# Optimization experiments

Measured on AMD Instinct MI355X. Metric: run time of the kernel, lower is better.

The kernel has to match this reference:

```python
import jax, jax.numpy as jnp
import numpy as np

N_NODES = 10000
N_EDGES = 160000
IN_CH = 1030
HID = 256
HEADS = 4
OUT_CH = 49
NEG_SLOPE = 0.2
EPS = 1e-5


def setup_inputs() -> dict:
    key = jax.random.key(0)
    ks = jax.random.split(key, 20)
    HC = HID * HEADS  # 1024
    inp = {
        "x": jax.random.normal(ks[0], (N_NODES, IN_CH), dtype=jnp.float32),
        "edge_index": jax.random.randint(ks[1], (2, N_EDGES), 0, N_NODES, dtype=jnp.int64),
        # conv1 (GATv2): lin_l (source), lin_r (target), att, out bias
        "c1_wl": jax.random.normal(ks[2], (IN_CH, HC), dtype=jnp.float32) * 0.03,
        "c1_bl": jnp.zeros((HC,), dtype=jnp.float32),
        "c1_wr": jax.random.normal(ks[3], (IN_CH, HC), dtype=jnp.float32) * 0.03,
        "c1_br": jnp.zeros((HC,), dtype=jnp.float32),
        "c1_att": jax.random.normal(ks[4], (HEADS, HID), dtype=jnp.float32) * 0.06,
        "c1_bias": jnp.zeros((HC,), dtype=jnp.float32),
        # norm1 (per-node LayerNorm over channels)
        "ln1_w": jnp.ones((HC,), dtype=jnp.float32),
        "ln1_b": jnp.zeros((HC,), dtype=jnp.float32),
        # conv2
        "c2_wl": jax.random.normal(ks[5], (HC, HC), dtype=jnp.float32) * 0.03,
        "c2_bl": jnp.zeros((HC,), dtype=jnp.float32),
        "c2_wr": jax.random.normal(ks[6], (HC, HC), dtype=jnp.float32) * 0.03,
        "c2_br": jnp.zeros((HC,), dtype=jnp.float32),
        "c2_att": jax.random.normal(ks[7], (HEADS, HID), dtype=jnp.float32) * 0.06,
        "c2_bias": jnp.zeros((HC,), dtype=jnp.float32),
        # norm2
        "ln2_w": jnp.ones((HC,), dtype=jnp.float32),
        "ln2_b": jnp.zeros((HC,), dtype=jnp.float32),
        # classifier: Linear(HC, HID) -> ELU -> Linear(HID, OUT_CH)
        "cls_w1": jax.random.normal(ks[8], (HC, HID), dtype=jnp.float32) * 0.03,
        "cls_b1": jnp.zeros((HID,), dtype=jnp.float32),
        "cls_w2": jax.random.normal(ks[9], (HID, OUT_CH), dtype=jnp.float32) * 0.06,
        "cls_b2": jnp.zeros((OUT_CH,), dtype=jnp.float32),
    }
    return inp


def gatv2_conv(x, src, dst, wl, bl, wr, br, att, bias, n_nodes):
    """PyG GATv2Conv, concat heads. src/dst include self loops."""
    H, C = att.shape
    xl = (x @ wl + bl).reshape(-1, H, C)  # source transform [N,H,C]
    xr = (x @ wr + br).reshape(-1, H, C)  # target transform [N,H,C]
    m = xl[src] + xr[dst]                  # [E,H,C] gather + add
    e = jnp.einsum("ehc,hc->eh", jax.nn.leaky_relu(m, NEG_SLOPE), att)  # [E,H]
    # segment softmax over destination node
    emax = jax.ops.segment_max(e, dst, num_segments=n_nodes)
    p = jnp.exp(e - emax[dst])
    denom = jax.ops.segment_sum(p, dst, num_segments=n_nodes)
    alpha = p / (denom[dst] + 1e-16)       # [E,H]
    out = jax.ops.segment_sum(xl[src] * alpha[:, :, None], dst, num_segments=n_nodes)
    return out.reshape(n_nodes, H * C) + bias


def layer_norm(x, w, b):
    mu = jnp.mean(x, axis=-1, keepdims=True)
    var = jnp.var(x, axis=-1, keepdims=True)
    return (x - mu) / jnp.sqrt(var + EPS) * w + b


def reference(x, edge_index, c1_wl, c1_bl, c1_wr, c1_br, c1_att, c1_bias,
              ln1_w, ln1_b, c2_wl, c2_bl, c2_wr, c2_br, c2_att, c2_bias,
              ln2_w, ln2_b, cls_w1, cls_b1, cls_w2, cls_b2):
    n = x.shape[0]
    loops = jnp.arange(n, dtype=edge_index.dtype)
    src = jnp.concatenate([edge_index[0], loops])  # add_self_loops=True
    dst = jnp.concatenate([edge_index[1], loops])

    h = gatv2_conv(x, src, dst, c1_wl, c1_bl, c1_wr, c1_br, c1_att, c1_bias, n)
    h = jax.nn.elu(layer_norm(h, ln1_w, ln1_b))
    # dropout: identity at inference
    h = gatv2_conv(h, src, dst, c2_wl, c2_bl, c2_wr, c2_br, c2_att, c2_bias, n)
    h = jax.nn.elu(layer_norm(h, ln2_w, ln2_b))
    h = jax.nn.elu(h @ cls_w1 + cls_b1)
    return h @ cls_w2 + cls_b2  # [N, 49]
```

## Files before the change

### kernel.cpp

```cpp
#include <hip/hip_runtime.h>
#include <stdint.h>

#define N_NODES 10000
#define N_EDGES 160000
#define E_TOT   170000
#define IN_CH   1030
#define HC      1024
#define OUT_CH  49
#define NEG_SLOPE 0.2f
#define LN_EPS 1e-5f

#define MPAD  10112
#define K1PAD 1088

typedef __attribute__((ext_vector_type(8))) __bf16 bf16x8;
typedef __attribute__((ext_vector_type(4))) float floatx4;
typedef __attribute__((ext_vector_type(2))) float floatx2;

static __device__ __forceinline__ unsigned short f2bf(float f) {
  union { float f; uint32_t u; } v; v.f = f;
  uint32_t u = v.u;
  u += 0x7fffu + ((u >> 16) & 1u);
  return (unsigned short)(u >> 16);
}
static __device__ __forceinline__ floatx2 unpk2(uint32_t u) {
  union { uint32_t i; float f; } a, b;
  a.i = u << 16; b.i = u & 0xffff0000u;
  floatx2 r; r.x = a.f; r.y = b.f; return r;
}
static __device__ __forceinline__ floatx2 max2(floatx2 a, floatx2 b) {
  floatx2 r; r.x = fmaxf(a.x, b.x); r.y = fmaxf(a.y, b.y); return r;
}


__global__ void cast_x_kernel(const float* __restrict__ x, unsigned short* __restrict__ xa) {
  int idx = blockIdx.x * 256 + threadIdx.x;
  if (idx >= N_NODES * K1PAD) return;
  int m = idx / K1PAD, k = idx - m * K1PAD;
  float v = (k < IN_CH) ? x[m * IN_CH + k] : 0.f;
  xa[idx] = f2bf(v);
}

__global__ void transpose_cast_kernel(const float* __restrict__ wa, const float* __restrict__ wb,
                                      int split, int lda, int ldb,
                                      int Kvalid, int Kout, unsigned short* __restrict__ out) {
  __shared__ float tile[32][33];
  int n0 = blockIdx.x * 32, k0 = blockIdx.y * 32;
  int tx = threadIdx.x, ty = threadIdx.y;
#pragma unroll
  for (int i = 0; i < 4; i++) {
    int k = k0 + ty + i * 8;
    int n = n0 + tx;
    float v = 0.f;
    if (k < Kvalid) v = (n < split) ? wa[(size_t)k * lda + n] : wb[(size_t)k * ldb + (n - split)];
    tile[ty + i * 8][tx] = v;
  }
  __syncthreads();
#pragma unroll
  for (int i = 0; i < 4; i++) {
    int n = n0 + ty + i * 8;
    int k = k0 + tx;
    out[(size_t)n * Kout + k] = f2bf(tile[tx][ty + i * 8]);
  }
}

__global__ void w2t_kernel(const float* __restrict__ w2, float* __restrict__ out) {
  int o = blockIdx.x;
  int k = threadIdx.x;
  out[o * 256 + k] = w2[k * OUT_CH + o];
}


__global__ void count_kernel(const int* __restrict__ dstArr, int* __restrict__ counts) {
  int e = blockIdx.x * 256 + threadIdx.x;
  if (e >= E_TOT) return;
  int d = (e < N_EDGES) ? dstArr[e] : (e - N_EDGES);
  atomicAdd(&counts[d], 1);
}

__global__ __launch_bounds__(256) void scan_kernel(const int* __restrict__ counts,
                                                   int* __restrict__ rstart) {
  __shared__ int sm[256];
  int t = threadIdx.x;
  int b0 = t * 40;
  int b1 = b0 + 40; if (b1 > N_NODES) b1 = N_NODES; if (b0 > N_NODES) b0 = N_NODES;
  int s = 0;
  for (int i = b0; i < b1; i++) s += counts[i];
  sm[t] = s; __syncthreads();
  for (int st = 1; st < 256; st <<= 1) {
    int add = (t >= st) ? sm[t - st] : 0;
    __syncthreads();
    sm[t] += add;
    __syncthreads();
  }
  int run = sm[t] - s;
  for (int i = b0; i < b1; i++) { rstart[i] = run; run += counts[i]; }
  if (t == 255) rstart[N_NODES] = run;
}

__global__ void scatter_kernel(const int* __restrict__ srcArr, const int* __restrict__ dstArr,
                               const int* __restrict__ row_start,
                               int* __restrict__ cursor, int* __restrict__ csrsrc) {
  int e = blockIdx.x * 256 + threadIdx.x;
  if (e >= E_TOT) return;
  int d, sv;
  if (e < N_EDGES) { d = dstArr[e]; sv = srcArr[e]; }
  else { d = e - N_EDGES; sv = d; }
  int pos = atomicAdd(&cursor[d], 1);
  csrsrc[row_start[d] + pos] = sv;
}

template <int MODE>
__global__ __launch_bounds__(256) void gemm_bf16(
    const unsigned short* __restrict__ A, const unsigned short* __restrict__ Bt,
    float* __restrict__ Cf, unsigned short* __restrict__ Cb,
    const float* __restrict__ blo, const float* __restrict__ bhi,
    int M, int K, int ldc, int bsplit)
{
  __shared__ __align__(16) unsigned short As[128 * 64];
  __shared__ __align__(16) unsigned short Bs[128 * 64];
  const int t = threadIdx.x;
  const int w = t >> 6, lane = t & 63;
  const int tile_n = blockIdx.x * 128, tile_m = blockIdx.y * 128;

  floatx4 acc[4][4] = {};

  const int q = w * 64 + lane;
  const int row0 = q >> 3;
  const int gj = (q & 7) ^ (row0 & 7);
  const unsigned short* gA0 = A  + (size_t)(tile_m + row0) * K + gj * 8;
  const unsigned short* gB0 = Bt + (size_t)(tile_n + row0) * K + gj * 8;

  const int wm = (w >> 1) * 64, wn = (w & 1) * 64;
  const int lrow = lane & 15, cg0 = (lane >> 4);
  const int sw = lrow & 7;

  for (int k0 = 0; k0 < K; k0 += 64) {
#pragma unroll
    for (int p = 0; p < 4; p++) {
      __builtin_amdgcn_global_load_lds(
          (const __attribute__((address_space(1))) void*)(gA0 + (size_t)p * 32 * K),
          (__attribute__((address_space(3))) void*)(As + p * 2048 + w * 512), 16, 0, 0);
      __builtin_amdgcn_global_load_lds(
          (const __attribute__((address_space(1))) void*)(gB0 + (size_t)p * 32 * K),
          (__attribute__((address_space(3))) void*)(Bs + p * 2048 + w * 512), 16, 0, 0);
    }
    gA0 += 64; gB0 += 64;
    __syncthreads();
#pragma unroll
    for (int h = 0; h < 2; h++) {
      const int sc = (h * 4 + cg0) ^ sw;
      bf16x8 a[4], b[4];
#pragma unroll
      for (int mi = 0; mi < 4; mi++)
        a[mi] = *(const bf16x8*)(As + (wm + mi * 16 + lrow) * 64 + sc * 8);
#pragma unroll
      for (int ni = 0; ni < 4; ni++)
        b[ni] = *(const bf16x8*)(Bs + (wn + ni * 16 + lrow) * 64 + sc * 8);
#pragma unroll
      for (int mi = 0; mi < 4; mi++)
#pragma unroll
        for (int ni = 0; ni < 4; ni++)
          acc[mi][ni] = __builtin_amdgcn_mfma_f32_16x16x32_bf16(a[mi], b[ni], acc[mi][ni], 0, 0, 0);
    }
    __syncthreads();
  }

  const int rbase = (lane >> 4) * 4;
#pragma unroll
  for (int mi = 0; mi < 4; mi++) {
#pragma unroll
    for (int r = 0; r < 4; r++) {
      int m = tile_m + wm + mi * 16 + rbase + r;
      if (m >= M) continue;
#pragma unroll
      for (int ni = 0; ni < 4; ni++) {
        int n = tile_n + wn + ni * 16 + lrow;
        float v = acc[mi][ni][r] + (n < bsplit ? blo[n] : bhi[n - bsplit]);
        if (MODE == 0) {
          Cf[(size_t)m * ldc + n] = v;
        } else if (MODE == 1) {
          Cf[(size_t)m * ldc + n] = v > 0.f ? v : expm1f(v);
        } else {
          Cb[(size_t)m * 2048 + n] = f2bf(v);
        }
      }
    }
  }
}


__global__ __launch_bounds__(256) void gat_ln_kernel(
    const unsigned short* __restrict__ xlr,
    const float* __restrict__ att,
    const int* __restrict__ csrsrc, const int* __restrict__ rstart,
    const float* __restrict__ bias,
    const float* __restrict__ lnw, const float* __restrict__ lnb,
    unsigned short* __restrict__ out)
{
  const int d = blockIdx.x;
  const int t = threadIdx.x;
  const int lane = t & 63, wv = t >> 6;
  const int c = wv * 256 + lane * 4;

  uint2 xru = *(const uint2*)(xlr + (size_t)d * 2048 + 1024 + c);
  floatx2 xrA = unpk2(xru.x), xrB = unpk2(xru.y);
  float4 aw4 = *(const float4*)(att + c);
  floatx2 awA; awA.x = aw4.x; awA.y = aw4.y;
  floatx2 awB; awB.x = aw4.z; awB.y = aw4.w;
  const unsigned short* xbase = xlr + c;

  int start = rstart[d], deg = rstart[d + 1] - start;

  float m = -3.0e38f, l = 0.f;
  floatx2 accA = {0.f, 0.f}, accB = {0.f, 0.f};

  int i = 0;
  for (; i + 2 <= deg; i += 2) {
    int s0 = csrsrc[start + i], s1 = csrsrc[start + i + 1];
    uint2 u0 = *(const uint2*)(xbase + (size_t)s0 * 2048);
    uint2 u1 = *(const uint2*)(xbase + (size_t)s1 * 2048);
    floatx2 x0A = unpk2(u0.x), x0B = unpk2(u0.y);
    floatx2 x1A = unpk2(u1.x), x1B = unpk2(u1.y);
    floatx2 t0A = x0A + xrA, t0B = x0B + xrB;
    floatx2 t1A = x1A + xrA, t1B = x1B + xrB;
    floatx2 l0A = max2(t0A, t0A * NEG_SLOPE), l0B = max2(t0B, t0B * NEG_SLOPE);
    floatx2 l1A = max2(t1A, t1A * NEG_SLOPE), l1B = max2(t1B, t1B * NEG_SLOPE);
    floatx2 P0 = l0A * awA; P0 += l0B * awB;
    floatx2 P1 = l1A * awA; P1 += l1B * awB;
    float p0 = P0.x + P0.y, p1 = P1.x + P1.y;
#pragma unroll
    for (int mm = 32; mm >= 1; mm >>= 1) {
      p0 += __shfl_xor(p0, mm, 64);
      p1 += __shfl_xor(p1, mm, 64);
    }
    float mx = fmaxf(p0, p1);
    if (mx > m) {
      float sc = __expf(m - mx);
      floatx2 scv; scv.x = sc; scv.y = sc;
      accA *= scv; accB *= scv; l *= sc;
      m = mx;
    }
    float pe0 = __expf(p0 - m), pe1 = __expf(p1 - m);
    floatx2 pe0v; pe0v.x = pe0; pe0v.y = pe0;
    floatx2 pe1v; pe1v.x = pe1; pe1v.y = pe1;
    accA += x0A * pe0v; accA += x1A * pe1v;
    accB += x0B * pe0v; accB += x1B * pe1v;
    l += pe0 + pe1;
  }
  if (i < deg) {
    int s0 = csrsrc[start + i];
    uint2 u0 = *(const uint2*)(xbase + (size_t)s0 * 2048);
    floatx2 x0A = unpk2(u0.x), x0B = unpk2(u0.y);
    floatx2 t0A = x0A + xrA, t0B = x0B + xrB;
    floatx2 l0A = max2(t0A, t0A * NEG_SLOPE), l0B = max2(t0B, t0B * NEG_SLOPE);
    floatx2 P0 = l0A * awA; P0 += l0B * awB;
    float p0 = P0.x + P0.y;
#pragma unroll
    for (int mm = 32; mm >= 1; mm >>= 1) p0 += __shfl_xor(p0, mm, 64);
    if (p0 > m) {
      float sc = __expf(m - p0);
      floatx2 scv; scv.x = sc; scv.y = sc;
      accA *= scv; accB *= scv; l *= sc;
      m = p0;
    }
    float pe0 = __expf(p0 - m);
    floatx2 pe0v; pe0v.x = pe0; pe0v.y = pe0;
    accA += x0A * pe0v;
    accB += x0B * pe0v;
    l += pe0;
  }

  float rd = 1.f / (l + 1e-16f);
  float4 bv = *(const float4*)(bias + c);
  float o0 = accA.x * rd + bv.x, o1 = accA.y * rd + bv.y;
  float o2 = accB.x * rd + bv.z, o3 = accB.y * rd + bv.w;

  __shared__ float ws1[4], ws2[4];
  float s1 = o0 + o1 + o2 + o3;
  float s2 = o0 * o0 + o1 * o1 + o2 * o2 + o3 * o3;
#pragma unroll
  for (int mm = 32; mm >= 1; mm >>= 1) {
    s1 += __shfl_xor(s1, mm, 64);
    s2 += __shfl_xor(s2, mm, 64);
  }
  if (lane == 0) { ws1[wv] = s1; ws2[wv] = s2; }
  __syncthreads();
  float mean = (ws1[0] + ws1[1] + ws1[2] + ws1[3]) * (1.f / 1024.f);
  float var  = (ws2[0] + ws2[1] + ws2[2] + ws2[3]) * (1.f / 1024.f) - mean * mean;
  float rstd = rsqrtf(var + LN_EPS);
  float4 wv4 = *(const float4*)(lnw + c);
  float4 bb  = *(const float4*)(lnb + c);
  float z0 = (o0 - mean) * rstd * wv4.x + bb.x; z0 = z0 > 0.f ? z0 : expm1f(z0);
  float z1 = (o1 - mean) * rstd * wv4.y + bb.y; z1 = z1 > 0.f ? z1 : expm1f(z1);
  float z2 = (o2 - mean) * rstd * wv4.z + bb.z; z2 = z2 > 0.f ? z2 : expm1f(z2);
  float z3 = (o3 - mean) * rstd * wv4.w + bb.w; z3 = z3 > 0.f ? z3 : expm1f(z3);
  ushort4 u;
  u.x = f2bf(z0); u.y = f2bf(z1); u.z = f2bf(z2); u.w = f2bf(z3);
  *(ushort4*)(out + (size_t)d * 1024 + c) = u;
}


__global__ __launch_bounds__(64) void cls2_kernel(
    const float* __restrict__ h3, const float* __restrict__ w2t,
    const float* __restrict__ b2, float* __restrict__ out)
{
  __shared__ float row[256];
  int node = blockIdx.x, t = threadIdx.x;
  *(float4*)(row + t * 4) = *(const float4*)(h3 + (size_t)node * 256 + t * 4);
  __syncthreads();
  if (t < OUT_CH) {
    const float* wr = w2t + t * 256;
    float acc = b2[t];
#pragma unroll 4
    for (int k = 0; k < 256; k += 4) {
      float4 a = *(const float4*)(row + k);
      float4 wv = *(const float4*)(wr + k);
      acc += a.x * wv.x + a.y * wv.y + a.z * wv.z + a.w * wv.w;
    }
    out[node * OUT_CH + t] = acc;
  }
}


extern "C" void kernel_launch(void* const* d_in, const int* in_sizes, int n_in,
                              void* d_out, int out_size, void* d_ws, size_t ws_size,
                              hipStream_t stream)
{
  const float* x       = (const float*)d_in[0];
  const int*   ei      = (const int*)d_in[1];
  const float* c1_wl   = (const float*)d_in[2];
  const float* c1_bl   = (const float*)d_in[3];
  const float* c1_wr   = (const float*)d_in[4];
  const float* c1_br   = (const float*)d_in[5];
  const float* c1_att  = (const float*)d_in[6];
  const float* c1_bias = (const float*)d_in[7];
  const float* ln1_w   = (const float*)d_in[8];
  const float* ln1_b   = (const float*)d_in[9];
  const float* c2_wl   = (const float*)d_in[10];
  const float* c2_bl   = (const float*)d_in[11];
  const float* c2_wr   = (const float*)d_in[12];
  const float* c2_br   = (const float*)d_in[13];
  const float* c2_att  = (const float*)d_in[14];
  const float* c2_bias = (const float*)d_in[15];
  const float* ln2_w   = (const float*)d_in[16];
  const float* ln2_b   = (const float*)d_in[17];
  const float* cls_w1  = (const float*)d_in[18];
  const float* cls_b1  = (const float*)d_in[19];
  const float* cls_w2  = (const float*)d_in[20];
  const float* cls_b2  = (const float*)d_in[21];

  const int* srcArr = ei;
  const int* dstArr = ei + N_EDGES;

  char* ws = (char*)d_ws;
  size_t off = 0;
  auto alloc = [&](size_t bytes) { void* p = ws + off; off += (bytes + 255) & ~(size_t)255; return p; };
  unsigned short* xa      = (unsigned short*)alloc((size_t)MPAD * K1PAD * 2);
  unsigned short* wt1     = (unsigned short*)alloc((size_t)2048 * K1PAD * 2);
  unsigned short* wt2     = (unsigned short*)alloc((size_t)2048 * 1024 * 2);
  unsigned short* wtc1    = (unsigned short*)alloc((size_t)256 * 1024 * 2);
  float*          w2t     = (float*)alloc((size_t)OUT_CH * 256 * 4);
  unsigned short* xlr     = (unsigned short*)alloc((size_t)N_NODES * 2048 * 2);
  float*          h3      = (float*)alloc((size_t)N_NODES * 256 * 4);
  unsigned short* hb      = (unsigned short*)alloc((size_t)MPAD * 1024 * 2);
  int*            counts  = (int*)alloc(N_NODES * 4);
  int*            cursor  = (int*)alloc(N_NODES * 4);
  int*            rstart  = (int*)alloc((N_NODES + 1) * 4);
  int*            csrsrc  = (int*)alloc(E_TOT * 4);
  (void)in_sizes; (void)n_in; (void)out_size; (void)ws_size;

  hipMemsetAsync(counts, 0, N_NODES * 4, stream);
  hipMemsetAsync(cursor, 0, N_NODES * 4, stream);

  cast_x_kernel<<<(N_NODES * K1PAD + 255) / 256, 256, 0, stream>>>(x, xa);
  transpose_cast_kernel<<<dim3(64, 34), dim3(32, 8), 0, stream>>>(c1_wl, c1_wr, 1024, 1024, 1024, IN_CH, K1PAD, wt1);
  transpose_cast_kernel<<<dim3(64, 32), dim3(32, 8), 0, stream>>>(c2_wl, c2_wr, 1024, 1024, 1024, 1024, 1024, wt2);
  transpose_cast_kernel<<<dim3(8, 32), dim3(32, 8), 0, stream>>>(cls_w1, cls_w1, 256, 256, 256, 1024, 1024, wtc1);
  w2t_kernel<<<OUT_CH, 256, 0, stream>>>(cls_w2, w2t);

  count_kernel<<<(E_TOT + 255) / 256, 256, 0, stream>>>(dstArr, counts);
  scan_kernel<<<1, 256, 0, stream>>>(counts, rstart);
  scatter_kernel<<<(E_TOT + 255) / 256, 256, 0, stream>>>(srcArr, dstArr, rstart, cursor, csrsrc);

  gemm_bf16<2><<<dim3(16, 79), 256, 0, stream>>>(xa, wt1, nullptr, xlr, c1_bl, c1_br, N_NODES, K1PAD, 0, 1024);
  gat_ln_kernel<<<N_NODES, 256, 0, stream>>>(xlr, c1_att, csrsrc, rstart, c1_bias, ln1_w, ln1_b, hb);

  gemm_bf16<2><<<dim3(16, 79), 256, 0, stream>>>(hb, wt2, nullptr, xlr, c2_bl, c2_br, N_NODES, 1024, 0, 1024);
  gat_ln_kernel<<<N_NODES, 256, 0, stream>>>(xlr, c2_att, csrsrc, rstart, c2_bias, ln2_w, ln2_b, hb);

  gemm_bf16<1><<<dim3(2, 79), 256, 0, stream>>>(hb, wtc1, h3, nullptr, cls_b1, cls_b1, N_NODES, 1024, 256, 1024);
  cls2_kernel<<<N_NODES, 64, 0, stream>>>(h3, w2t, cls_b2, (float*)d_out);
}
```

Measured before the change: 534.2 us.

## Split GAT aggregation across half-waves with 16-byte loads and merge softmax states

The GAT attention kernel now has each 32-lane half-wave handle alternate edges, with every lane loading 8 bf16 channels (16 bytes) instead of 4. Each half keeps its own online-softmax state, and the two are merged with cross-half shuffles at the end. The per-edge reduction also becomes branchless and uses 5 shuffle steps instead of 6. Separately, the two memsets of the CSR counters are folded into the cast kernel to cut launch overhead. The trade-off is more registers per lane and half the lanes sitting idle during the LayerNorm store.

```diff
diff --git a/kernel.cpp b/kernel.cpp
--- a/kernel.cpp
+++ b/kernel.cpp
@@ -31,10 +31,15 @@
 static __device__ __forceinline__ floatx2 max2(floatx2 a, floatx2 b) {
   floatx2 r; r.x = fmaxf(a.x, b.x); r.y = fmaxf(a.y, b.y); return r;
 }
-
-
-__global__ void cast_x_kernel(const float* __restrict__ x, unsigned short* __restrict__ xa) {
+static __device__ __forceinline__ uint32_t pk2bf(float a, float b) {
+  return (uint32_t)f2bf(a) | ((uint32_t)f2bf(b) << 16);
+}
+
+
+__global__ void cast_x_kernel(const float* __restrict__ x, unsigned short* __restrict__ xa,
+                              int* __restrict__ counts, int* __restrict__ cursor) {
   int idx = blockIdx.x * 256 + threadIdx.x;
+  if (idx < N_NODES) { counts[idx] = 0; cursor[idx] = 0; }
   if (idx >= N_NODES * K1PAD) return;
   int m = idx / K1PAD, k = idx - m * K1PAD;
   float v = (k < IN_CH) ? x[m * IN_CH + k] : 0.f;
@@ -201,86 +206,71 @@
   const int d = blockIdx.x;
   const int t = threadIdx.x;
   const int lane = t & 63, wv = t >> 6;
-  const int c = wv * 256 + lane * 4;
-
-  uint2 xru = *(const uint2*)(xlr + (size_t)d * 2048 + 1024 + c);
-  floatx2 xrA = unpk2(xru.x), xrB = unpk2(xru.y);
-  float4 aw4 = *(const float4*)(att + c);
-  floatx2 awA; awA.x = aw4.x; awA.y = aw4.y;
-  floatx2 awB; awB.x = aw4.z; awB.y = aw4.w;
-  const unsigned short* xbase = xlr + c;
+  const int half = lane >> 5, j = lane & 31;
+  const int c = wv * 256 + j * 8;
+
+  uint4 xru = *(const uint4*)(xlr + (size_t)d * 2048 + 1024 + c);
+  floatx2 xr2[4] = {unpk2(xru.x), unpk2(xru.y), unpk2(xru.z), unpk2(xru.w)};
+  float4 awa = *(const float4*)(att + c);
+  float4 awb = *(const float4*)(att + c + 4);
+  floatx2 aw2[4];
+  aw2[0].x = awa.x; aw2[0].y = awa.y; aw2[1].x = awa.z; aw2[1].y = awa.w;
+  aw2[2].x = awb.x; aw2[2].y = awb.y; aw2[3].x = awb.z; aw2[3].y = awb.w;
 
   int start = rstart[d], deg = rstart[d + 1] - start;
 
   float m = -3.0e38f, l = 0.f;
-  floatx2 accA = {0.f, 0.f}, accB = {0.f, 0.f};
-
-  int i = 0;
-  for (; i + 2 <= deg; i += 2) {
-    int s0 = csrsrc[start + i], s1 = csrsrc[start + i + 1];
-    uint2 u0 = *(const uint2*)(xbase + (size_t)s0 * 2048);
-    uint2 u1 = *(const uint2*)(xbase + (size_t)s1 * 2048);
-    floatx2 x0A = unpk2(u0.x), x0B = unpk2(u0.y);
-    floatx2 x1A = unpk2(u1.x), x1B = unpk2(u1.y);
-    floatx2 t0A = x0A + xrA, t0B = x0B + xrB;
-    floatx2 t1A = x1A + xrA, t1B = x1B + xrB;
-    floatx2 l0A = max2(t0A, t0A * NEG_SLOPE), l0B = max2(t0B, t0B * NEG_SLOPE);
-    floatx2 l1A = max2(t1A, t1A * NEG_SLOPE), l1B = max2(t1B, t1B * NEG_SLOPE);
-    floatx2 P0 = l0A * awA; P0 += l0B * awB;
-    floatx2 P1 = l1A * awA; P1 += l1B * awB;
-    float p0 = P0.x + P0.y, p1 = P1.x + P1.y;
-#pragma unroll
-    for (int mm = 32; mm >= 1; mm >>= 1) {
-      p0 += __shfl_xor(p0, mm, 64);
-      p1 += __shfl_xor(p1, mm, 64);
-    }
-    float mx = fmaxf(p0, p1);
-    if (mx > m) {
-      float sc = __expf(m - mx);
-      floatx2 scv; scv.x = sc; scv.y = sc;
-      accA *= scv; accB *= scv; l *= sc;
-      m = mx;
-    }
-    float pe0 = __expf(p0 - m), pe1 = __expf(p1 - m);
-    floatx2 pe0v; pe0v.x = pe0; pe0v.y = pe0;
-    floatx2 pe1v; pe1v.x = pe1; pe1v.y = pe1;
-    accA += x0A * pe0v; accA += x1A * pe1v;
-    accB += x0B * pe0v; accB += x1B * pe1v;
-    l += pe0 + pe1;
-  }
-  if (i < deg) {
-    int s0 = csrsrc[start + i];
-    uint2 u0 = *(const uint2*)(xbase + (size_t)s0 * 2048);
-    floatx2 x0A = unpk2(u0.x), x0B = unpk2(u0.y);
-    floatx2 t0A = x0A + xrA, t0B = x0B + xrB;
-    floatx2 l0A = max2(t0A, t0A * NEG_SLOPE), l0B = max2(t0B, t0B * NEG_SLOPE);
-    floatx2 P0 = l0A * awA; P0 += l0B * awB;
-    float p0 = P0.x + P0.y;
-#pragma unroll
-    for (int mm = 32; mm >= 1; mm >>= 1) p0 += __shfl_xor(p0, mm, 64);
-    if (p0 > m) {
-      float sc = __expf(m - p0);
-      floatx2 scv; scv.x = sc; scv.y = sc;
-      accA *= scv; accB *= scv; l *= sc;
-      m = p0;
-    }
-    float pe0 = __expf(p0 - m);
-    floatx2 pe0v; pe0v.x = pe0; pe0v.y = pe0;
-    accA += x0A * pe0v;
-    accB += x0B * pe0v;
-    l += pe0;
-  }
-
-  float rd = 1.f / (l + 1e-16f);
-  float4 bv = *(const float4*)(bias + c);
-  float o0 = accA.x * rd + bv.x, o1 = accA.y * rd + bv.y;
-  float o2 = accB.x * rd + bv.z, o3 = accB.y * rd + bv.w;
+  floatx2 acc2[4] = {};
+
+  for (int i = half; i < deg; i += 2) {
+    int s = csrsrc[start + i];
+    uint4 u = *(const uint4*)(xlr + (size_t)s * 2048 + c);
+    floatx2 xs[4] = {unpk2(u.x), unpk2(u.y), unpk2(u.z), unpk2(u.w)};
+    floatx2 P = {0.f, 0.f};
+#pragma unroll
+    for (int q = 0; q < 4; q++) {
+      floatx2 tt = xs[q] + xr2[q];
+      floatx2 lr = max2(tt, tt * NEG_SLOPE);
+      P += lr * aw2[q];
+    }
+    float p = P.x + P.y;
+#pragma unroll
+    for (int mm = 16; mm >= 1; mm >>= 1) p += __shfl_xor(p, mm, 64);
+    float mn = fmaxf(m, p);
+    float sc = __expf(m - mn), pe = __expf(p - mn);
+    floatx2 scv; scv.x = sc; scv.y = sc;
+    floatx2 pev; pev.x = pe; pev.y = pe;
+#pragma unroll
+    for (int q = 0; q < 4; q++) acc2[q] = acc2[q] * scv + xs[q] * pev;
+    l = l * sc + pe;
+    m = mn;
+  }
+
+  float mo = __shfl_xor(m, 32, 64);
+  float lo = __shfl_xor(l, 32, 64);
+  float M = fmaxf(m, mo);
+  float ea = __expf(m - M), eb = __expf(mo - M);
+  float L = l * ea + lo * eb + 1e-16f;
+  float rd = 1.f / L;
+  float o[8];
+#pragma unroll
+  for (int q = 0; q < 4; q++) {
+    float ax = acc2[q].x, ay = acc2[q].y;
+    float bx = __shfl_xor(ax, 32, 64), by = __shfl_xor(ay, 32, 64);
+    o[2 * q]     = (ax * ea + bx * eb) * rd;
+    o[2 * q + 1] = (ay * ea + by * eb) * rd;
+  }
+  float4 bva = *(const float4*)(bias + c);
+  float4 bvb = *(const float4*)(bias + c + 4);
+  o[0] += bva.x; o[1] += bva.y; o[2] += bva.z; o[3] += bva.w;
+  o[4] += bvb.x; o[5] += bvb.y; o[6] += bvb.z; o[7] += bvb.w;
 
   __shared__ float ws1[4], ws2[4];
-  float s1 = o0 + o1 + o2 + o3;
-  float s2 = o0 * o0 + o1 * o1 + o2 * o2 + o3 * o3;
-#pragma unroll
-  for (int mm = 32; mm >= 1; mm >>= 1) {
+  float s1 = 0.f, s2 = 0.f;
+#pragma unroll
+  for (int q = 0; q < 8; q++) { s1 += o[q]; s2 += o[q] * o[q]; }
+#pragma unroll
+  for (int mm = 16; mm >= 1; mm >>= 1) {
     s1 += __shfl_xor(s1, mm, 64);
     s2 += __shfl_xor(s2, mm, 64);
   }
@@ -289,15 +279,27 @@
   float mean = (ws1[0] + ws1[1] + ws1[2] + ws1[3]) * (1.f / 1024.f);
   float var  = (ws2[0] + ws2[1] + ws2[2] + ws2[3]) * (1.f / 1024.f) - mean * mean;
   float rstd = rsqrtf(var + LN_EPS);
-  float4 wv4 = *(const float4*)(lnw + c);
-  float4 bb  = *(const float4*)(lnb + c);
-  float z0 = (o0 - mean) * rstd * wv4.x + bb.x; z0 = z0 > 0.f ? z0 : expm1f(z0);
-  float z1 = (o1 - mean) * rstd * wv4.y + bb.y; z1 = z1 > 0.f ? z1 : expm1f(z1);
-  float z2 = (o2 - mean) * rstd * wv4.z + bb.z; z2 = z2 > 0.f ? z2 : expm1f(z2);
-  float z3 = (o3 - mean) * rstd * wv4.w + bb.w; z3 = z3 > 0.f ? z3 : expm1f(z3);
-  ushort4 u;
-  u.x = f2bf(z0); u.y = f2bf(z1); u.z = f2bf(z2); u.w = f2bf(z3);
-  *(ushort4*)(out + (size_t)d * 1024 + c) = u;
+
+  if (half == 0) {
+    float4 wva = *(const float4*)(lnw + c);
+    float4 wvb = *(const float4*)(lnw + c + 4);
+    float4 bba = *(const float4*)(lnb + c);
+    float4 bbb = *(const float4*)(lnb + c + 4);
+    float wz[8] = {wva.x, wva.y, wva.z, wva.w, wvb.x, wvb.y, wvb.z, wvb.w};
+    float bz[8] = {bba.x, bba.y, bba.z, bba.w, bbb.x, bbb.y, bbb.z, bbb.w};
+    float z[8];
+#pragma unroll
+    for (int q = 0; q < 8; q++) {
+      float v = (o[q] - mean) * rstd * wz[q] + bz[q];
+      z[q] = v > 0.f ? v : expm1f(v);
+    }
+    uint4 st;
+    st.x = pk2bf(z[0], z[1]);
+    st.y = pk2bf(z[2], z[3]);
+    st.z = pk2bf(z[4], z[5]);
+    st.w = pk2bf(z[6], z[7]);
+    *(uint4*)(out + (size_t)d * 1024 + c) = st;
+  }
 }
 
 
@@ -370,10 +372,7 @@
   int*            csrsrc  = (int*)alloc(E_TOT * 4);
   (void)in_sizes; (void)n_in; (void)out_size; (void)ws_size;
 
-  hipMemsetAsync(counts, 0, N_NODES * 4, stream);
-  hipMemsetAsync(cursor, 0, N_NODES * 4, stream);
-
-  cast_x_kernel<<<(N_NODES * K1PAD + 255) / 256, 256, 0, stream>>>(x, xa);
+  cast_x_kernel<<<(N_NODES * K1PAD + 255) / 256, 256, 0, stream>>>(x, xa, counts, cursor);
   transpose_cast_kernel<<<dim3(64, 34), dim3(32, 8), 0, stream>>>(c1_wl, c1_wr, 1024, 1024, 1024, IN_CH, K1PAD, wt1);
   transpose_cast_kernel<<<dim3(64, 32), dim3(32, 8), 0, stream>>>(c2_wl, c2_wr, 1024, 1024, 1024, 1024, 1024, wt2);
   transpose_cast_kernel<<<dim3(8, 32), dim3(32, 8), 0, stream>>>(cls_w1, cls_w1, 256, 256, 256, 1024, 1024, wtc1);
```

After: 550.1 us. 3.0% more time.
